# Kernel optimization log

Measured on AMD Instinct MI355X. Metric: run time of the kernel, lower is better.

The kernel has to match this reference:

```python
import jax, jax.numpy as jnp
import numpy as np

N = 100000; E = 800000; IN_DIM = 32; HID = 64; HEADS = 4; HEAD_DIM = HID // HEADS; L = 3; G = 128

def setup_inputs() -> dict:
    key = jax.random.key(0)
    ks = jax.random.split(key, 12)
    nrm = lambda k, shape: jax.random.normal(k, shape, jnp.float32) * 0.05
    return {
        "x": jax.random.normal(ks[0], (N, IN_DIM), jnp.float32),
        "edge_index": jax.random.randint(ks[1], (2, E), 0, N),
        "edge_attr": jax.random.normal(ks[2], (E, 1), jnp.float32),
        "batch": jnp.sort(jax.random.randint(ks[3], (N,), 0, G)),
        "in_W": nrm(ks[4], (IN_DIM, HID)), "in_b": jnp.zeros((HID,), jnp.float32),
        "in_ln_g": jnp.ones((HID,), jnp.float32), "in_ln_b": jnp.zeros((HID,), jnp.float32),
        "W_qkv": nrm(ks[5], (L, 3, HID, HID)), "b_qkv": jnp.zeros((L, 3, HID), jnp.float32),
        "W_edge": nrm(ks[6], (L, 1, HID)),
        "W_skip": nrm(ks[7], (L, HID, HID)), "b_skip": jnp.zeros((L, HID), jnp.float32),
        "W_beta": nrm(ks[8], (L, 3 * HID)),
        "ln_g": jnp.ones((L, HID), jnp.float32), "ln_b": jnp.zeros((L, HID), jnp.float32),
        "r1_W": nrm(ks[9], (2 * HID, HID)), "r1_b": jnp.zeros((HID,), jnp.float32),
        "r2_W": nrm(ks[10], (HID, HID // 2)), "r2_b": jnp.zeros((HID // 2,), jnp.float32),
        "r3_W": nrm(ks[11], (HID // 2, 1)), "r3_b": jnp.zeros((1,), jnp.float32),
    }

def _layer_norm(x, g, b, eps=1e-5):
    mu = x.mean(-1, keepdims=True)
    var = ((x - mu) ** 2).mean(-1, keepdims=True)
    return (x - mu) * jax.lax.rsqrt(var + eps) * g + b

def _gelu(x):
    return jax.nn.gelu(x, approximate=False)  # matches torch F.gelu default (erf)

def _forward(x, edge_attr, in_W, in_b, in_ln_g, in_ln_b, W_qkv, b_qkv, W_edge,
             W_skip, b_skip, W_beta, ln_g, ln_b, r1_W, r1_b, r2_W, r2_b, r3_W, r3_b,
             edge_index, batch):
    src, dst = edge_index[0], edge_index[1]  # message flows src -> dst
    n = x.shape[0]
    h = _layer_norm(_gelu(x @ in_W + in_b), in_ln_g, in_ln_b)
    scale = 1.0 / jnp.sqrt(jnp.float32(HEAD_DIM))
    for l in range(L):
        res = h
        q = (h @ W_qkv[l, 0] + b_qkv[l, 0]).reshape(n, HEADS, HEAD_DIM)
        k = (h @ W_qkv[l, 1] + b_qkv[l, 1]).reshape(n, HEADS, HEAD_DIM)
        v = (h @ W_qkv[l, 2] + b_qkv[l, 2]).reshape(n, HEADS, HEAD_DIM)
        e = (edge_attr @ W_edge[l]).reshape(-1, HEADS, HEAD_DIM)  # [E,H,C]
        ke = k[src] + e
        alpha = jnp.einsum("ehc,ehc->eh", q[dst], ke) * scale      # [E,H]
        amax = jax.ops.segment_max(alpha, dst, num_segments=n)
        ex = jnp.exp(alpha - amax[dst])
        den = jax.ops.segment_sum(ex, dst, num_segments=n)
        alpha = ex / (den[dst] + 1e-16)                            # PyG softmax eps
        msg = alpha[..., None] * (v[src] + e)
        out = jax.ops.segment_sum(msg, dst, num_segments=n).reshape(n, HID)
        x_r = h @ W_skip[l] + b_skip[l]
        beta = jax.nn.sigmoid(jnp.concatenate([out, x_r, out - x_r], -1) @ W_beta[l])  # [N]
        out = beta[:, None] * x_r + (1.0 - beta[:, None]) * out
        h = _layer_norm(_gelu(out) + res, ln_g[l], ln_b[l])
    cnt = jax.ops.segment_sum(jnp.ones((n,), h.dtype), batch, num_segments=G)
    gmean = jax.ops.segment_sum(h, batch, num_segments=G) / jnp.maximum(cnt, 1.0)[:, None]
    gmax = jax.ops.segment_max(h, batch, num_segments=G)
    rep = jnp.concatenate([gmean, gmax], -1)  # [G, 2*HID]
    rep = _gelu(rep @ r1_W + r1_b)
    rep = _gelu(rep @ r2_W + r2_b)
    return (rep @ r3_W + r3_b).reshape(-1)

def reference(x, edge_index, edge_attr, batch, in_W, in_b, in_ln_g, in_ln_b,
              W_qkv, b_qkv, W_edge, W_skip, b_skip, W_beta, ln_g, ln_b,
              r1_W, r1_b, r2_W, r2_b, r3_W, r3_b):
    return _forward(x, edge_attr, in_W, in_b, in_ln_g, in_ln_b, W_qkv, b_qkv, W_edge,
                    W_skip, b_skip, W_beta, ln_g, ln_b, r1_W, r1_b, r2_W, r2_b, r3_W, r3_b,
                    edge_index, batch)
```

## Files before the change

### kernel.cpp

```cpp
#include <hip/hip_runtime.h>
#include <hip/hip_fp16.h>
#include <math.h>
#include <float.h>

#define LAYERS 3
#define NGRAPH 128
#define NPB 1024
#define NBMAX 256

typedef __attribute__((ext_vector_type(8))) short bf16x8;
typedef __attribute__((ext_vector_type(4))) float f32x4;

union bfr { int4 i; bf16x8 b; };

__device__ __forceinline__ float gelu_f(float x) {
    return 0.5f * x * (1.0f + erff(x * 0.70710678118654752440f));
}

template <int CTRL, int RMASK>
__device__ __forceinline__ float dpp_add(float x) {
    int t = __builtin_amdgcn_update_dpp(0, __float_as_int(x), CTRL, RMASK, 0xF, false);
    return x + __int_as_float(t);
}

__device__ __forceinline__ float sum16(float v) {
    v = dpp_add<0xB1, 0xF>(v);
    v = dpp_add<0x4E, 0xF>(v);
    v = dpp_add<0x141, 0xF>(v);
    v = dpp_add<0x140, 0xF>(v);
    return v;
}

__device__ __forceinline__ unsigned int f2mono(float f) {
    unsigned int u = __float_as_uint(f);
    return (u & 0x80000000u) ? ~u : (u | 0x80000000u);
}
__device__ __forceinline__ float mono2f(unsigned int u) {
    return (u & 0x80000000u) ? __uint_as_float(u ^ 0x80000000u)
                             : __uint_as_float(~u);
}

__device__ __forceinline__ float2 h2f2(int bits) {
    __half2 h = *reinterpret_cast<__half2*>(&bits);
    return __half22float2(h);
}

__device__ __forceinline__ void cvt_frag(const float4& f0, const float4& f1,
                                         bf16x8& hi, bf16x8& lo) {
    float ff[8] = {f0.x, f0.y, f0.z, f0.w, f1.x, f1.y, f1.z, f1.w};
#pragma unroll
    for (int j = 0; j < 8; j++) {
        unsigned u = __float_as_uint(ff[j]);
        hi[j] = (short)(u >> 16);
        float hf = __uint_as_float(u & 0xFFFF0000u);
        lo[j] = (short)(__float_as_uint(ff[j] - hf) >> 16);
    }
}

__device__ __forceinline__ f32x4 mm3(const bf16x8& ahi, const bf16x8& alo,
                                     const int4* __restrict__ pk, int tile,
                                     int lane, f32x4 acc) {
    bfr bh, bl;
    bh.i = pk[tile * 128 + lane];
    bl.i = pk[tile * 128 + 64 + lane];
    acc = __builtin_amdgcn_mfma_f32_16x16x32_bf16(alo, bh.b, acc, 0, 0, 0);
    acc = __builtin_amdgcn_mfma_f32_16x16x32_bf16(ahi, bl.b, acc, 0, 0, 0);
    acc = __builtin_amdgcn_mfma_f32_16x16x32_bf16(ahi, bh.b, acc, 0, 0, 0);
    return acc;
}

__device__ __forceinline__ int kv_idx(int m, int cc) {
    return (cc >> 2) * 8 + (m - 1) * 4 + (cc & 3);
}

__global__ __launch_bounds__(256) void k_cvt(
    const float* __restrict__ in_W, const float* __restrict__ W_skip,
    const float* __restrict__ W_qkv, int4* __restrict__ pk_in,
    int4* __restrict__ pk_skip, int4* __restrict__ pk_qkv) {
    int w = (blockIdx.x * 256 + threadIdx.x) >> 6;
    if (w >= 100) return;
    int lane = threadIdx.x & 63;
    const float* src;
    int4* dst;
    int kt, jt, qkvmode = 0;
    if (w < 4) {
        kt = 0; jt = w;
        src = in_W;
        dst = pk_in + w * 128;
    } else {
        int l = (w - 4) >> 5, r = (w - 4) & 31;
        if (r < 8) {
            kt = r & 1; jt = r >> 1;
            src = W_skip + l * 4096;
            dst = pk_skip + (l * 8 + r) * 128;
        } else {
            int tq = r - 8;
            kt = tq & 1; jt = tq >> 1;
            src = W_qkv + l * 12288;
            dst = pk_qkv + (l * 24 + tq) * 128;
            qkvmode = 1;
        }
    }
    int c = jt * 16 + (lane & 15);
    int koff = kt * 32 + (lane >> 4) * 8;
    unsigned hi[8], lo[8];
#pragma unroll
    for (int j = 0; j < 8; j++) {
        int k = koff + j;
        float f = qkvmode ? src[(c >> 6) * 4096 + k * 64 + (c & 63)]
                          : src[k * 64 + c];
        unsigned u = __float_as_uint(f);
        hi[j] = u >> 16;
        float hf = __uint_as_float(u & 0xFFFF0000u);
        lo[j] = __float_as_uint(f - hf) >> 16;
    }
    int4 H, L;
    H.x = hi[0] | (hi[1] << 16); H.y = hi[2] | (hi[3] << 16);
    H.z = hi[4] | (hi[5] << 16); H.w = hi[6] | (hi[7] << 16);
    L.x = lo[0] | (lo[1] << 16); L.y = lo[2] | (lo[3] << 16);
    L.z = lo[4] | (lo[5] << 16); L.w = lo[6] | (lo[7] << 16);
    dst[lane] = H;
    dst[64 + lane] = L;
}

__global__ __launch_bounds__(256) void k_hist(const int* __restrict__ dst,
                                              int* __restrict__ deg, int E) {
    int e = blockIdx.x * 256 + threadIdx.x;
    if (e < E) atomicAdd(&deg[dst[e]], 1);
}

__global__ __launch_bounds__(256) void k_scan1(const int* __restrict__ deg,
                                               int* __restrict__ excl,
                                               int* __restrict__ bsum, int n) {
    __shared__ int s[256];
    int t = threadIdx.x;
    int i = blockIdx.x * 256 + t;
    int v = (i < n) ? deg[i] : 0;
    s[t] = v;
    __syncthreads();
    for (int off = 1; off < 256; off <<= 1) {
        int a = (t >= off) ? s[t - off] : 0;
        __syncthreads();
        s[t] += a;
        __syncthreads();
    }
    if (i < n) excl[i] = s[t] - v;
    if (t == 255) bsum[blockIdx.x] = s[255];
}

__global__ __launch_bounds__(512) void k_scan2(int* __restrict__ bsum, int nb) {
    __shared__ int s[512];
    int t = threadIdx.x;
    int v = (t < nb) ? bsum[t] : 0;
    s[t] = v;
    __syncthreads();
    for (int off = 1; off < 512; off <<= 1) {
        int a = (t >= off) ? s[t - off] : 0;
        __syncthreads();
        s[t] += a;
        __syncthreads();
    }
    if (t < nb) bsum[t] = s[t] - v;
}

__global__ __launch_bounds__(256) void k_scan3(const int* __restrict__ excl,
                                               const int* __restrict__ bsum,
                                               int* __restrict__ row,
                                               int* __restrict__ cursor,
                                               int* __restrict__ gcurb,
                                               int n, int E) {
    int i = blockIdx.x * 256 + threadIdx.x;
    if (i < n) {
        int r = excl[i] + bsum[blockIdx.x];
        row[i] = r;
        cursor[i] = r;
        if ((i & (NPB - 1)) == 0) gcurb[i >> 10] = r;
    }
    if (blockIdx.x == 0 && threadIdx.x == 0) row[n] = E;
}

__global__ __launch_bounds__(256) void k_bucket(
    const int* __restrict__ src, const int* __restrict__ dst,
    const float* __restrict__ ea, int* __restrict__ gcurb,
    int2* __restrict__ mid, int E, int nbkt) {
    __shared__ int cnt[NBMAX], base_[NBMAX];
    int tile = blockIdx.x * 4096;
    for (int i = threadIdx.x; i < nbkt; i += 256) cnt[i] = 0;
    __syncthreads();
    int d[16];
#pragma unroll
    for (int j = 0; j < 16; j++) {
        int e = tile + j * 256 + threadIdx.x;
        d[j] = -1;
        if (e < E) {
            d[j] = dst[e];
            atomicAdd(&cnt[d[j] >> 10], 1);
        }
    }
    __syncthreads();
    for (int i = threadIdx.x; i < nbkt; i += 256) {
        base_[i] = atomicAdd(&gcurb[i], cnt[i]);
        cnt[i] = 0;
    }
    __syncthreads();
#pragma unroll
    for (int j = 0; j < 16; j++) {
        int e = tile + j * 256 + threadIdx.x;
        if (e < E) {
            int b = d[j] >> 10;
            int p = base_[b] + atomicAdd(&cnt[b], 1);
            mid[p] = make_int2(src[e] | ((d[j] & (NPB - 1)) << 20),
                               __float_as_int(ea[e]));
        }
    }
}

__global__ __launch_bounds__(256) void k_local(
    const int* __restrict__ row, int* __restrict__ cursor,
    const int2* __restrict__ mid, int2* __restrict__ ep, int n) {
    int b = blockIdx.x;
    int n0 = b << 10;
    int n1 = min(n, n0 + NPB);
    int ebeg = row[n0], eend = row[n1];
    for (int e = ebeg + blockIdx.y * 256 + threadIdx.x; e < eend;
         e += 256 * gridDim.y) {
        int2 m = mid[e];
        int dn = n0 + ((m.x >> 20) & (NPB - 1));
        int p = atomicAdd(&cursor[dn], 1);
        ep[p] = make_int2(m.x & 0xFFFFF, m.y);
    }
}

__global__ __launch_bounds__(64) void k_in_qkv(
    const float* __restrict__ x, const int4* __restrict__ pk_in,
    const float* __restrict__ b, const float* __restrict__ g,
    const float* __restrict__ be, const int4* __restrict__ pk_qkv,
    const float* __restrict__ bn, float* __restrict__ h,
    __half* __restrict__ q, __half* __restrict__ kvout, int n) {
    __shared__ float ldsA[1088];
    int lane = threadIdx.x;
    int nb = blockIdx.x * 16;
    if (nb >= n) return;
    int g16 = lane >> 4, c16 = lane & 15;
    bool rowok = (nb + c16) < n;
    int arow = min(nb + c16, n - 1);
    const float* xp = x + (size_t)arow * 32 + g16 * 8;
    float4 f0 = *(const float4*)xp;
    float4 f1 = *(const float4*)(xp + 4);
    bf16x8 ahi, alo;
    cvt_frag(f0, f1, ahi, alo);
    float gv[4][4];
#pragma unroll
    for (int jt = 0; jt < 4; jt++) {
        f32x4 a = {0.f, 0.f, 0.f, 0.f};
        a = mm3(ahi, alo, pk_in, jt, lane, a);
        float bb = b[jt * 16 + c16];
#pragma unroll
        for (int r = 0; r < 4; r++) gv[jt][r] = gelu_f(a[r] + bb);
    }
    float gl[4], bel[4];
#pragma unroll
    for (int jt = 0; jt < 4; jt++) {
        gl[jt] = g[jt * 16 + c16];
        bel[jt] = be[jt * 16 + c16];
    }
    float hreg[4][4];
#pragma unroll
    for (int r = 0; r < 4; r++) {
        float s = gv[0][r] + gv[1][r] + gv[2][r] + gv[3][r];
        float mu = sum16(s) * (1.0f / 64.0f);
        float vs = 0.f;
#pragma unroll
        for (int jt = 0; jt < 4; jt++) {
            float d = gv[jt][r] - mu;
            vs += d * d;
        }
        float var = sum16(vs) * (1.0f / 64.0f);
        float rs = rsqrtf(var + 1e-5f);
#pragma unroll
        for (int jt = 0; jt < 4; jt++)
            hreg[jt][r] = (gv[jt][r] - mu) * rs * gl[jt] + bel[jt];
    }
#pragma unroll
    for (int jt = 0; jt < 4; jt++)
#pragma unroll
        for (int r = 0; r < 4; r++)
            ldsA[(g16 * 4 + r) * 68 + jt * 16 + c16] = hreg[jt][r];
    if (rowok) {
        float* hp = h + (size_t)(nb + c16) * 64 + g16 * 16;
#pragma unroll
        for (int i = 0; i < 4; i++)
            *(float4*)(hp + i * 4) = *(const float4*)&ldsA[c16 * 68 + g16 * 16 + i * 4];
    }
    bf16x8 qahi[2], qalo[2];
#pragma unroll
    for (int kt = 0; kt < 2; kt++) {
        const float* lp = &ldsA[c16 * 68 + kt * 32 + g16 * 8];
        float4 t0 = *(const float4*)lp;
        float4 t1 = *(const float4*)(lp + 4);
        cvt_frag(t0, t1, qahi[kt], qalo[kt]);
    }
#pragma unroll
    for (int jt = 0; jt < 12; jt++) {
        f32x4 a = {0.f, 0.f, 0.f, 0.f};
#pragma unroll
        for (int kt = 0; kt < 2; kt++) a = mm3(qahi[kt], qalo[kt], pk_qkv, jt * 2 + kt, lane, a);
        int c = jt * 16 + c16;
        float bias = bn[c];
        int m = c >> 6, cc = c & 63;
#pragma unroll
        for (int r = 0; r < 4; r++) {
            int nd = nb + g16 * 4 + r;
            if (nd < n) {
                float val = a[r] + bias;
                if (m == 0) q[(size_t)nd * 64 + cc] = __float2half(val);
                else kvout[(size_t)nd * 128 + kv_idx(m, cc)] = __float2half(val);
            }
        }
    }
}

__global__ __launch_bounds__(256) void k_attn(
    const __half* __restrict__ q, const __half* __restrict__ kv,
    const int* __restrict__ row, const int2* __restrict__ ep,
    const float* __restrict__ We, float* __restrict__ out, int n) {
    int lane = threadIdx.x & 63;
    int node = blockIdx.x * 4 + (threadIdx.x >> 6);
    if (node >= n) return;
    int g = lane >> 4;
    int c16 = lane & 15;
    int2 qb = *(const int2*)(q + (size_t)node * 64 + c16 * 4);
    float2 q01 = h2f2(qb.x), q23 = h2f2(qb.y);
    float4 wv = *(const float4*)(We + c16 * 4);
    int beg = row[node], end = row[node + 1];
    float den = 0.f;
    float4 acc = {0.f, 0.f, 0.f, 0.f};
    for (int pos = beg; pos < end; pos += 8) {
        int idx0 = pos + g, idx1 = pos + 4 + g;
        bool v0 = idx0 < end, v1 = idx1 < end;
        int2 pr0 = ep[v0 ? idx0 : beg];
        int2 pr1 = ep[v1 ? idx1 : beg];
        float a0 = __int_as_float(pr0.y), a1 = __int_as_float(pr1.y);
        int4 kb0 = *(const int4*)(kv + (size_t)pr0.x * 128 + c16 * 8);
        int4 kb1 = *(const int4*)(kv + (size_t)pr1.x * 128 + c16 * 8);
        {
            float2 k01 = h2f2(kb0.x), k23 = h2f2(kb0.y);
            float2 v01 = h2f2(kb0.z), v23 = h2f2(kb0.w);
            float p = q01.x * fmaf(a0, wv.x, k01.x) + q01.y * fmaf(a0, wv.y, k01.y) +
                      q23.x * fmaf(a0, wv.z, k23.x) + q23.y * fmaf(a0, wv.w, k23.y);
            p = dpp_add<0xB1, 0xF>(p);
            p = dpp_add<0x4E, 0xF>(p);
            float ex = v0 ? __expf(fminf(p * 0.25f, 60.f)) : 0.f;
            den += ex;
            acc.x = fmaf(ex, fmaf(a0, wv.x, v01.x), acc.x);
            acc.y = fmaf(ex, fmaf(a0, wv.y, v01.y), acc.y);
            acc.z = fmaf(ex, fmaf(a0, wv.z, v23.x), acc.z);
            acc.w = fmaf(ex, fmaf(a0, wv.w, v23.y), acc.w);
        }
        {
            float2 k01 = h2f2(kb1.x), k23 = h2f2(kb1.y);
            float2 v01 = h2f2(kb1.z), v23 = h2f2(kb1.w);
            float p = q01.x * fmaf(a1, wv.x, k01.x) + q01.y * fmaf(a1, wv.y, k01.y) +
                      q23.x * fmaf(a1, wv.z, k23.x) + q23.y * fmaf(a1, wv.w, k23.y);
            p = dpp_add<0xB1, 0xF>(p);
            p = dpp_add<0x4E, 0xF>(p);
            float ex = v1 ? __expf(fminf(p * 0.25f, 60.f)) : 0.f;
            den += ex;
            acc.x = fmaf(ex, fmaf(a1, wv.x, v01.x), acc.x);
            acc.y = fmaf(ex, fmaf(a1, wv.y, v01.y), acc.y);
            acc.z = fmaf(ex, fmaf(a1, wv.z, v23.x), acc.z);
            acc.w = fmaf(ex, fmaf(a1, wv.w, v23.y), acc.w);
        }
    }
#pragma unroll
    for (int mask = 16; mask <= 32; mask <<= 1) {
        den += __shfl_xor(den, mask, 64);
        acc.x += __shfl_xor(acc.x, mask, 64);
        acc.y += __shfl_xor(acc.y, mask, 64);
        acc.z += __shfl_xor(acc.z, mask, 64);
        acc.w += __shfl_xor(acc.w, mask, 64);
    }
    if (g == 0) {
        float inv = 1.0f / (den + 1e-16f);
        float4 o = {acc.x * inv, acc.y * inv, acc.z * inv, acc.w * inv};
        *(float4*)(out + (size_t)node * 64 + c16 * 4) = o;
    }
}

template <int DO_QKV>
__global__ __launch_bounds__(64) void k_node_qkv(
    float* __restrict__ h, const float* __restrict__ o_in,
    const int4* __restrict__ pk_skip, const float* __restrict__ bs,
    const float* __restrict__ Wb, const float* __restrict__ lg,
    const float* __restrict__ lb, const int4* __restrict__ pk_qkv,
    const float* __restrict__ bn, __half* __restrict__ q,
    __half* __restrict__ kvout, const int* __restrict__ batch,
    float* __restrict__ gsum, unsigned int* __restrict__ gmaxu,
    float* __restrict__ cnt, int n) {
    __shared__ float ldsA[1088];
    int lane = threadIdx.x;
    int nb = blockIdx.x * 16;
    if (nb >= n) return;
    int g16 = lane >> 4, c16 = lane & 15;
    bool rowok = (nb + c16) < n;
    int arow = min(nb + c16, n - 1);
    float4 hf[2][2];
#pragma unroll
    for (int kt = 0; kt < 2; kt++) {
        const float* hp = h + (size_t)arow * 64 + kt * 32 + g16 * 8;
        hf[kt][0] = *(const float4*)hp;
        hf[kt][1] = *(const float4*)(hp + 4);
    }
    float ov[4][4];
#pragma unroll
    for (int jt = 0; jt < 4; jt++)
#pragma unroll
        for (int r = 0; r < 4; r++) {
            int nd = min(nb + g16 * 4 + r, n - 1);
            ov[jt][r] = o_in[(size_t)nd * 64 + jt * 16 + c16];
        }
    bf16x8 ahi[2], alo[2];
#pragma unroll
    for (int kt = 0; kt < 2; kt++) {
        cvt_frag(hf[kt][0], hf[kt][1], ahi[kt], alo[kt]);
        *(float4*)&ldsA[c16 * 68 + kt * 32 + g16 * 8] = hf[kt][0];
        *(float4*)&ldsA[c16 * 68 + kt * 32 + g16 * 8 + 4] = hf[kt][1];
    }
    float xr[4][4];
#pragma unroll
    for (int jt = 0; jt < 4; jt++) {
        f32x4 a = {0.f, 0.f, 0.f, 0.f};
#pragma unroll
        for (int kt = 0; kt < 2; kt++) a = mm3(ahi[kt], alo[kt], pk_skip, jt * 2 + kt, lane, a);
        float bias = bs[jt * 16 + c16];
#pragma unroll
        for (int r = 0; r < 4; r++) xr[jt][r] = a[r] + bias;
    }
    float hold[4][4];
#pragma unroll
    for (int jt = 0; jt < 4; jt++)
#pragma unroll
        for (int r = 0; r < 4; r++)
            hold[jt][r] = ldsA[(g16 * 4 + r) * 68 + jt * 16 + c16];
    float wb0[4], wb1[4], wb2[4], lgv[4], lbv[4];
#pragma unroll
    for (int jt = 0; jt < 4; jt++) {
        int c = jt * 16 + c16;
        wb0[jt] = Wb[c]; wb1[jt] = Wb[64 + c]; wb2[jt] = Wb[128 + c];
        lgv[jt] = lg[c]; lbv[jt] = lb[c];
    }
    float hnew[4][4];
#pragma unroll
    for (int r = 0; r < 4; r++) {
        float cbs = 0.f;
#pragma unroll
        for (int jt = 0; jt < 4; jt++)
            cbs += ov[jt][r] * wb0[jt] + xr[jt][r] * wb1[jt] +
                   (ov[jt][r] - xr[jt][r]) * wb2[jt];
        float cb = sum16(cbs);
        float beta = 1.0f / (1.0f + expf(-cb));
        float gvr[4], s = 0.f;
#pragma unroll
        for (int jt = 0; jt < 4; jt++) {
            float o2 = fmaf(beta, xr[jt][r] - ov[jt][r], ov[jt][r]);
            gvr[jt] = gelu_f(o2) + hold[jt][r];
            s += gvr[jt];
        }
        float mu = sum16(s) * (1.0f / 64.0f);
        float vs = 0.f;
#pragma unroll
        for (int jt = 0; jt < 4; jt++) {
            float d = gvr[jt] - mu;
            vs += d * d;
        }
        float var = sum16(vs) * (1.0f / 64.0f);
        float rs = rsqrtf(var + 1e-5f);
#pragma unroll
        for (int jt = 0; jt < 4; jt++)
            hnew[jt][r] = (gvr[jt] - mu) * rs * lgv[jt] + lbv[jt];
    }
    if (DO_QKV) {
#pragma unroll
        for (int jt = 0; jt < 4; jt++)
#pragma unroll
            for (int r = 0; r < 4; r++)
                ldsA[(g16 * 4 + r) * 68 + jt * 16 + c16] = hnew[jt][r];
        if (rowok) {
            float* hp = h + (size_t)(nb + c16) * 64 + g16 * 16;
#pragma unroll
            for (int i = 0; i < 4; i++)
                *(float4*)(hp + i * 4) = *(const float4*)&ldsA[c16 * 68 + g16 * 16 + i * 4];
        }
        bf16x8 qahi[2], qalo[2];
#pragma unroll
        for (int kt = 0; kt < 2; kt++) {
            const float* lp = &ldsA[c16 * 68 + kt * 32 + g16 * 8];
            float4 t0 = *(const float4*)lp;
            float4 t1 = *(const float4*)(lp + 4);
            cvt_frag(t0, t1, qahi[kt], qalo[kt]);
        }
#pragma unroll
        for (int jt = 0; jt < 12; jt++) {
            f32x4 a = {0.f, 0.f, 0.f, 0.f};
#pragma unroll
            for (int kt = 0; kt < 2; kt++) a = mm3(qahi[kt], qalo[kt], pk_qkv, jt * 2 + kt, lane, a);
            int c = jt * 16 + c16;
            float bias = bn[c];
            int m = c >> 6, cc = c & 63;
#pragma unroll
            for (int r = 0; r < 4; r++) {
                int nd = nb + g16 * 4 + r;
                if (nd < n) {
                    float val = a[r] + bias;
                    if (m == 0) q[(size_t)nd * 64 + cc] = __float2half(val);
                    else kvout[(size_t)nd * 128 + kv_idx(m, cc)] = __float2half(val);
                }
            }
        }
    } else {
        int gid[4];
        int g0 = batch[nb];
        bool ok = (nb + 15 < n);
#pragma unroll
        for (int r = 0; r < 4; r++)
            gid[r] = batch[min(nb + g16 * 4 + r, n - 1)];
        bool uni = ok && __all(gid[0] == g0 && gid[1] == g0 &&
                               gid[2] == g0 && gid[3] == g0);
        if (uni) {
            float s[4], mx[4];
#pragma unroll
            for (int jt = 0; jt < 4; jt++) {
                s[jt] = hnew[jt][0] + hnew[jt][1] + hnew[jt][2] + hnew[jt][3];
                mx[jt] = fmaxf(fmaxf(hnew[jt][0], hnew[jt][1]),
                               fmaxf(hnew[jt][2], hnew[jt][3]));
            }
#pragma unroll
            for (int mask = 16; mask <= 32; mask <<= 1) {
#pragma unroll
                for (int jt = 0; jt < 4; jt++) {
                    s[jt] += __shfl_xor(s[jt], mask, 64);
                    mx[jt] = fmaxf(mx[jt], __shfl_xor(mx[jt], mask, 64));
                }
            }
            if (g16 == 0) {
#pragma unroll
                for (int jt = 0; jt < 4; jt++) {
                    int ch = jt * 16 + c16;
                    atomicAdd(&gsum[g0 * 64 + ch], s[jt]);
                    atomicMax(&gmaxu[g0 * 64 + ch], f2mono(mx[jt]));
                }
            }
            if (lane == 0) atomicAdd(&cnt[g0], 16.0f);
        } else {
#pragma unroll
            for (int r = 0; r < 4; r++) {
                int nd = nb + g16 * 4 + r;
                if (nd >= n) continue;
#pragma unroll
                for (int jt = 0; jt < 4; jt++) {
                    int ch = jt * 16 + c16;
                    atomicAdd(&gsum[gid[r] * 64 + ch], hnew[jt][r]);
                    atomicMax(&gmaxu[gid[r] * 64 + ch], f2mono(hnew[jt][r]));
                }
                if (c16 == 0) atomicAdd(&cnt[gid[r]], 1.0f);
            }
        }
    }
}

__global__ void k_final(const float* __restrict__ gsum,
                        const unsigned int* __restrict__ gmax,
                        const float* __restrict__ cnt,
                        const float* __restrict__ W1, const float* __restrict__ b1,
                        const float* __restrict__ W2, const float* __restrict__ b2,
                        const float* __restrict__ W3, const float* __restrict__ b3,
                        float* __restrict__ out) {
    int g = blockIdx.x;
    int lane = threadIdx.x;
    __shared__ float rep[128];
    __shared__ float t1[64];
    __shared__ float t2[32];
    float c = fmaxf(cnt[g], 1.0f);
    rep[lane] = gsum[g * 64 + lane] / c;
    rep[64 + lane] = mono2f(gmax[g * 64 + lane]);
    __syncthreads();
    float a = b1[lane];
#pragma unroll 8
    for (int i = 0; i < 128; i++) a = fmaf(rep[i], W1[i * 64 + lane], a);
    t1[lane] = gelu_f(a);
    __syncthreads();
    if (lane < 32) {
        float a2 = b2[lane];
#pragma unroll 8
        for (int i = 0; i < 64; i++) a2 = fmaf(t1[i], W2[i * 32 + lane], a2);
        t2[lane] = gelu_f(a2);
    }
    __syncthreads();
    if (lane < 32) {
        float p = t2[lane] * W3[lane];
#pragma unroll
        for (int o = 16; o > 0; o >>= 1) p += __shfl_xor(p, o, 64);
        if (lane == 0) out[g] = p + b3[0];
    }
}

extern "C" void kernel_launch(void* const* d_in, const int* in_sizes, int n_in,
                              void* d_out, int out_size, void* d_ws,
                              size_t ws_size, hipStream_t stream) {
    const float* x      = (const float*)d_in[0];
    const int*   eidx   = (const int*)d_in[1];
    const float* ea     = (const float*)d_in[2];
    const int*   batch  = (const int*)d_in[3];
    const float* in_W   = (const float*)d_in[4];
    const float* in_b   = (const float*)d_in[5];
    const float* in_lng = (const float*)d_in[6];
    const float* in_lnb = (const float*)d_in[7];
    const float* W_qkv  = (const float*)d_in[8];
    const float* b_qkv  = (const float*)d_in[9];
    const float* W_edge = (const float*)d_in[10];
    const float* W_skip = (const float*)d_in[11];
    const float* b_skip = (const float*)d_in[12];
    const float* W_beta = (const float*)d_in[13];
    const float* ln_g   = (const float*)d_in[14];
    const float* ln_b   = (const float*)d_in[15];
    const float* r1_W   = (const float*)d_in[16];
    const float* r1_b   = (const float*)d_in[17];
    const float* r2_W   = (const float*)d_in[18];
    const float* r2_b   = (const float*)d_in[19];
    const float* r3_W   = (const float*)d_in[20];
    const float* r3_b   = (const float*)d_in[21];

    int n = in_sizes[0] / 32;
    int E = in_sizes[2];
    const int* src = eidx;
    const int* dst = eidx + E;

    char* ws = (char*)d_ws;
    size_t off = 0;
    auto alloc = [&](size_t bytes) -> void* {
        void* p = ws + off;
        off = (off + bytes + 255) & ~(size_t)255;
        return p;
    };
    float* h    = (float*)alloc((size_t)n * 64 * 4);
    __half* qh  = (__half*)alloc((size_t)n * 64 * 2);
    __half* kvh = (__half*)alloc((size_t)n * 128 * 2);
    float* oacc = (float*)alloc((size_t)n * 64 * 4);
    int* deg    = (int*)alloc((size_t)n * 4);
    int* excl   = (int*)alloc((size_t)n * 4);
    int* bsum   = (int*)alloc(512 * 4);
    int* row    = (int*)alloc((size_t)(n + 1) * 4);
    int* cursor = (int*)alloc((size_t)n * 4);
    int* gcurb  = (int*)alloc(NBMAX * 4);
    int2* mid   = (int2*)alloc((size_t)E * 8);
    int2* ep    = (int2*)alloc((size_t)E * 8);
    int4* pk_in   = (int4*)alloc(4 * 128 * 16);
    int4* pk_skip = (int4*)alloc(3 * 8 * 128 * 16);
    int4* pk_qkv  = (int4*)alloc((size_t)3 * 24 * 128 * 16);
    float* gsum = (float*)alloc((NGRAPH * 64 * 2 + NGRAPH) * 4);
    unsigned int* gmaxu = (unsigned int*)(gsum + NGRAPH * 64);
    float* cnt  = gsum + NGRAPH * 128;

    int nb4 = (n + 3) / 4;
    int nb16 = (n + 15) / 16;
    int nbs = (n + 255) / 256;
    int ebs = (E + 255) / 256;
    int nbkt = (n + NPB - 1) >> 10;

    k_cvt<<<25, 256, 0, stream>>>(in_W, W_skip, W_qkv, pk_in, pk_skip, pk_qkv);
    hipMemsetAsync(deg, 0, (size_t)n * 4, stream);
    hipMemsetAsync(gsum, 0, (NGRAPH * 64 * 2 + NGRAPH) * 4, stream);
    k_hist<<<ebs, 256, 0, stream>>>(dst, deg, E);
    k_scan1<<<nbs, 256, 0, stream>>>(deg, excl, bsum, n);
    k_scan2<<<1, 512, 0, stream>>>(bsum, nbs);
    k_scan3<<<nbs, 256, 0, stream>>>(excl, bsum, row, cursor, gcurb, n, E);
    k_bucket<<<(E + 4095) / 4096, 256, 0, stream>>>(src, dst, ea, gcurb, mid, E, nbkt);
    k_local<<<dim3(nbkt, 4), 256, 0, stream>>>(row, cursor, mid, ep, n);

    k_in_qkv<<<nb16, 64, 0, stream>>>(x, pk_in, in_b, in_lng, in_lnb,
                                      pk_qkv, b_qkv, h, qh, kvh, n);

    for (int l = 0; l < LAYERS; l++) {
        k_attn<<<nb4, 256, 0, stream>>>(qh, kvh, row, ep, W_edge + l * 64, oacc, n);
        if (l + 1 < LAYERS) {
            k_node_qkv<1><<<nb16, 64, 0, stream>>>(
                h, oacc, pk_skip + l * 8 * 128, b_skip + l * 64,
                W_beta + l * 192, ln_g + l * 64, ln_b + l * 64,
                pk_qkv + (size_t)(l + 1) * 24 * 128, b_qkv + (size_t)(l + 1) * 192,
                qh, kvh, nullptr, nullptr, nullptr, nullptr, n);
        } else {
            k_node_qkv<0><<<nb16, 64, 0, stream>>>(
                h, oacc, pk_skip + l * 8 * 128, b_skip + l * 64,
                W_beta + l * 192, ln_g + l * 64, ln_b + l * 64,
                nullptr, nullptr, nullptr, nullptr,
                batch, gsum, gmaxu, cnt, n);
        }
    }

    k_final<<<NGRAPH, 64, 0, stream>>>(gsum, gmaxu, cnt, r1_W, r1_b, r2_W, r2_b,
                                       r3_W, r3_b, (float*)d_out);
}
```

Baseline: 385.3 us.

## Stage packed weights in LDS and process four 16-node tiles per block

```diff
diff --git a/kernel.cpp b/kernel.cpp
--- a/kernel.cpp
+++ b/kernel.cpp
@@ -57,12 +57,12 @@
     }
 }
 
-__device__ __forceinline__ f32x4 mm3(const bf16x8& ahi, const bf16x8& alo,
-                                     const int4* __restrict__ pk, int tile,
-                                     int lane, f32x4 acc) {
+__device__ __forceinline__ f32x4 mm3l(const bf16x8& ahi, const bf16x8& alo,
+                                      const int4* wW, int tile, int lane,
+                                      f32x4 acc) {
     bfr bh, bl;
-    bh.i = pk[tile * 128 + lane];
-    bl.i = pk[tile * 128 + 64 + lane];
+    bh.i = wW[tile * 128 + lane];
+    bl.i = wW[tile * 128 + 64 + lane];
     acc = __builtin_amdgcn_mfma_f32_16x16x32_bf16(alo, bh.b, acc, 0, 0, 0);
     acc = __builtin_amdgcn_mfma_f32_16x16x32_bf16(ahi, bl.b, acc, 0, 0, 0);
     acc = __builtin_amdgcn_mfma_f32_16x16x32_bf16(ahi, bh.b, acc, 0, 0, 0);
@@ -231,90 +231,112 @@
     }
 }
 
-__global__ __launch_bounds__(64) void k_in_qkv(
+__global__ __launch_bounds__(256) void k_in_qkv(
     const float* __restrict__ x, const int4* __restrict__ pk_in,
     const float* __restrict__ b, const float* __restrict__ g,
     const float* __restrict__ be, const int4* __restrict__ pk_qkv,
     const float* __restrict__ bn, float* __restrict__ h,
     __half* __restrict__ q, __half* __restrict__ kvout, int n) {
-    __shared__ float ldsA[1088];
-    int lane = threadIdx.x;
-    int nb = blockIdx.x * 16;
-    if (nb >= n) return;
+    __shared__ float ldsA[4][1088];
+    __shared__ int4 wW[1536];
+    int lane = threadIdx.x & 63, wid = threadIdx.x >> 6, tid = threadIdx.x;
+    int nb = (blockIdx.x * 4 + wid) * 16;
+    bool active = nb < n;
     int g16 = lane >> 4, c16 = lane & 15;
-    bool rowok = (nb + c16) < n;
-    int arow = min(nb + c16, n - 1);
-    const float* xp = x + (size_t)arow * 32 + g16 * 8;
-    float4 f0 = *(const float4*)xp;
-    float4 f1 = *(const float4*)(xp + 4);
-    bf16x8 ahi, alo;
-    cvt_frag(f0, f1, ahi, alo);
-    float gv[4][4];
-#pragma unroll
-    for (int jt = 0; jt < 4; jt++) {
-        f32x4 a = {0.f, 0.f, 0.f, 0.f};
-        a = mm3(ahi, alo, pk_in, jt, lane, a);
-        float bb = b[jt * 16 + c16];
-#pragma unroll
-        for (int r = 0; r < 4; r++) gv[jt][r] = gelu_f(a[r] + bb);
-    }
-    float gl[4], bel[4];
-#pragma unroll
-    for (int jt = 0; jt < 4; jt++) {
-        gl[jt] = g[jt * 16 + c16];
-        bel[jt] = be[jt * 16 + c16];
-    }
-    float hreg[4][4];
-#pragma unroll
-    for (int r = 0; r < 4; r++) {
-        float s = gv[0][r] + gv[1][r] + gv[2][r] + gv[3][r];
-        float mu = sum16(s) * (1.0f / 64.0f);
-        float vs = 0.f;
+    bool rowok = active && (nb + c16) < n;
+    int arow = active ? min(nb + c16, n - 1) : 0;
+#pragma unroll
+    for (int i = 0; i < 2; i++) wW[tid + i * 256] = pk_in[tid + i * 256];
+    float4 f0 = {0,0,0,0}, f1 = {0,0,0,0};
+    if (active) {
+        const float* xp = x + (size_t)arow * 32 + g16 * 8;
+        f0 = *(const float4*)xp;
+        f1 = *(const float4*)(xp + 4);
+    }
+    __syncthreads();
+    bf16x8 qahi[2], qalo[2];
+    if (active) {
+        bf16x8 ahi, alo;
+        cvt_frag(f0, f1, ahi, alo);
+        float gv[4][4];
 #pragma unroll
         for (int jt = 0; jt < 4; jt++) {
-            float d = gv[jt][r] - mu;
-            vs += d * d;
-        }
-        float var = sum16(vs) * (1.0f / 64.0f);
-        float rs = rsqrtf(var + 1e-5f);
+            f32x4 a = {0.f, 0.f, 0.f, 0.f};
+            a = mm3l(ahi, alo, wW, jt, lane, a);
+            float bb = b[jt * 16 + c16];
+#pragma unroll
+            for (int r = 0; r < 4; r++) gv[jt][r] = gelu_f(a[r] + bb);
+        }
+        float gl[4], bel[4];
+#pragma unroll
+        for (int jt = 0; jt < 4; jt++) {
+            gl[jt] = g[jt * 16 + c16];
+            bel[jt] = be[jt * 16 + c16];
+        }
+        float hreg[4][4];
+#pragma unroll
+        for (int r = 0; r < 4; r++) {
+            float s = gv[0][r] + gv[1][r] + gv[2][r] + gv[3][r];
+            float mu = sum16(s) * (1.0f / 64.0f);
+            float vs = 0.f;
+#pragma unroll
+            for (int jt = 0; jt < 4; jt++) {
+                float d = gv[jt][r] - mu;
+                vs += d * d;
+            }
+            float var = sum16(vs) * (1.0f / 64.0f);
+            float rs = rsqrtf(var + 1e-5f);
+#pragma unroll
+            for (int jt = 0; jt < 4; jt++)
+                hreg[jt][r] = (gv[jt][r] - mu) * rs * gl[jt] + bel[jt];
+        }
 #pragma unroll
         for (int jt = 0; jt < 4; jt++)
-            hreg[jt][r] = (gv[jt][r] - mu) * rs * gl[jt] + bel[jt];
-    }
-#pragma unroll
-    for (int jt = 0; jt < 4; jt++)
-#pragma unroll
-        for (int r = 0; r < 4; r++)
-            ldsA[(g16 * 4 + r) * 68 + jt * 16 + c16] = hreg[jt][r];
-    if (rowok) {
-        float* hp = h + (size_t)(nb + c16) * 64 + g16 * 16;
-#pragma unroll
-        for (int i = 0; i < 4; i++)
-            *(float4*)(hp + i * 4) = *(const float4*)&ldsA[c16 * 68 + g16 * 16 + i * 4];
-    }
-    bf16x8 qahi[2], qalo[2];
-#pragma unroll
-    for (int kt = 0; kt < 2; kt++) {
-        const float* lp = &ldsA[c16 * 68 + kt * 32 + g16 * 8];
-        float4 t0 = *(const float4*)lp;
-        float4 t1 = *(const float4*)(lp + 4);
-        cvt_frag(t0, t1, qahi[kt], qalo[kt]);
-    }
-#pragma unroll
-    for (int jt = 0; jt < 12; jt++) {
-        f32x4 a = {0.f, 0.f, 0.f, 0.f};
-#pragma unroll
-        for (int kt = 0; kt < 2; kt++) a = mm3(qahi[kt], qalo[kt], pk_qkv, jt * 2 + kt, lane, a);
-        int c = jt * 16 + c16;
-        float bias = bn[c];
-        int m = c >> 6, cc = c & 63;
-#pragma unroll
-        for (int r = 0; r < 4; r++) {
-            int nd = nb + g16 * 4 + r;
-            if (nd < n) {
-                float val = a[r] + bias;
-                if (m == 0) q[(size_t)nd * 64 + cc] = __float2half(val);
-                else kvout[(size_t)nd * 128 + kv_idx(m, cc)] = __float2half(val);
+#pragma unroll
+            for (int r = 0; r < 4; r++)
+                ldsA[wid][(g16 * 4 + r) * 68 + jt * 16 + c16] = hreg[jt][r];
+        if (rowok) {
+            float* hp = h + (size_t)(nb + c16) * 64 + g16 * 16;
+#pragma unroll
+            for (int i = 0; i < 4; i++)
+                *(float4*)(hp + i * 4) =
+                    *(const float4*)&ldsA[wid][c16 * 68 + g16 * 16 + i * 4];
+        }
+#pragma unroll
+        for (int kt = 0; kt < 2; kt++) {
+            const float* lp = &ldsA[wid][c16 * 68 + kt * 32 + g16 * 8];
+            float4 t0 = *(const float4*)lp;
+            float4 t1 = *(const float4*)(lp + 4);
+            cvt_frag(t0, t1, qahi[kt], qalo[kt]);
+        }
+    }
+#pragma unroll
+    for (int half = 0; half < 2; half++) {
+        __syncthreads();
+#pragma unroll
+        for (int i = 0; i < 6; i++)
+            wW[tid + i * 256] = pk_qkv[half * 1536 + tid + i * 256];
+        __syncthreads();
+        if (active) {
+#pragma unroll
+            for (int j6 = 0; j6 < 6; j6++) {
+                int jt = half * 6 + j6;
+                f32x4 a = {0.f, 0.f, 0.f, 0.f};
+#pragma unroll
+                for (int kt = 0; kt < 2; kt++)
+                    a = mm3l(qahi[kt], qalo[kt], wW, j6 * 2 + kt, lane, a);
+                int c = jt * 16 + c16;
+                float bias = bn[c];
+                int m = c >> 6, cc = c & 63;
+#pragma unroll
+                for (int r = 0; r < 4; r++) {
+                    int nd = nb + g16 * 4 + r;
+                    if (nd < n) {
+                        float val = a[r] + bias;
+                        if (m == 0) q[(size_t)nd * 64 + cc] = __float2half(val);
+                        else kvout[(size_t)nd * 128 + kv_idx(m, cc)] = __float2half(val);
+                    }
+                }
             }
         }
     }
@@ -388,7 +410,7 @@
 }
 
 template <int DO_QKV>
-__global__ __launch_bounds__(64) void k_node_qkv(
+__global__ __launch_bounds__(256) void k_node_qkv(
     float* __restrict__ h, const float* __restrict__ o_in,
     const int4* __restrict__ pk_skip, const float* __restrict__ bs,
     const float* __restrict__ Wb, const float* __restrict__ lg,
@@ -397,127 +419,150 @@
     __half* __restrict__ kvout, const int* __restrict__ batch,
     float* __restrict__ gsum, unsigned int* __restrict__ gmaxu,
     float* __restrict__ cnt, int n) {
-    __shared__ float ldsA[1088];
-    int lane = threadIdx.x;
-    int nb = blockIdx.x * 16;
-    if (nb >= n) return;
+    __shared__ float ldsA[4][1088];
+    __shared__ int4 wW[1536];
+    int lane = threadIdx.x & 63, wid = threadIdx.x >> 6, tid = threadIdx.x;
+    int nb = (blockIdx.x * 4 + wid) * 16;
+    bool active = nb < n;
     int g16 = lane >> 4, c16 = lane & 15;
-    bool rowok = (nb + c16) < n;
-    int arow = min(nb + c16, n - 1);
-    float4 hf[2][2];
-#pragma unroll
-    for (int kt = 0; kt < 2; kt++) {
-        const float* hp = h + (size_t)arow * 64 + kt * 32 + g16 * 8;
-        hf[kt][0] = *(const float4*)hp;
-        hf[kt][1] = *(const float4*)(hp + 4);
-    }
+    bool rowok = active && (nb + c16) < n;
+    int arow = active ? min(nb + c16, n - 1) : 0;
+#pragma unroll
+    for (int i = 0; i < 4; i++) wW[tid + i * 256] = pk_skip[tid + i * 256];
+    float4 hf0 = {0,0,0,0}, hf1 = {0,0,0,0}, hf2 = {0,0,0,0}, hf3 = {0,0,0,0};
     float ov[4][4];
-#pragma unroll
-    for (int jt = 0; jt < 4; jt++)
+    if (active) {
+        const float* hp0 = h + (size_t)arow * 64 + g16 * 8;
+        hf0 = *(const float4*)hp0;
+        hf1 = *(const float4*)(hp0 + 4);
+        hf2 = *(const float4*)(hp0 + 32);
+        hf3 = *(const float4*)(hp0 + 36);
+#pragma unroll
+        for (int jt = 0; jt < 4; jt++)
+#pragma unroll
+            for (int r = 0; r < 4; r++) {
+                int nd = min(nb + g16 * 4 + r, n - 1);
+                ov[jt][r] = o_in[(size_t)nd * 64 + jt * 16 + c16];
+            }
+    }
+    __syncthreads();
+    float hnew[4][4];
+    bf16x8 qahi[2], qalo[2];
+    if (active) {
+        bf16x8 ahi[2], alo[2];
+        cvt_frag(hf0, hf1, ahi[0], alo[0]);
+        cvt_frag(hf2, hf3, ahi[1], alo[1]);
+        *(float4*)&ldsA[wid][c16 * 68 + g16 * 8] = hf0;
+        *(float4*)&ldsA[wid][c16 * 68 + g16 * 8 + 4] = hf1;
+        *(float4*)&ldsA[wid][c16 * 68 + 32 + g16 * 8] = hf2;
+        *(float4*)&ldsA[wid][c16 * 68 + 32 + g16 * 8 + 4] = hf3;
+        float xr[4][4];
+#pragma unroll
+        for (int jt = 0; jt < 4; jt++) {
+            f32x4 a = {0.f, 0.f, 0.f, 0.f};
+#pragma unroll
+            for (int kt = 0; kt < 2; kt++)
+                a = mm3l(ahi[kt], alo[kt], wW, jt * 2 + kt, lane, a);
+            float bias = bs[jt * 16 + c16];
+#pragma unroll
+            for (int r = 0; r < 4; r++) xr[jt][r] = a[r] + bias;
+        }
+        float hold[4][4];
+#pragma unroll
+        for (int jt = 0; jt < 4; jt++)
+#pragma unroll
+            for (int r = 0; r < 4; r++)
+                hold[jt][r] = ldsA[wid][(g16 * 4 + r) * 68 + jt * 16 + c16];
+        float wb0[4], wb1[4], wb2[4], lgv[4], lbv[4];
+#pragma unroll
+        for (int jt = 0; jt < 4; jt++) {
+            int c = jt * 16 + c16;
+            wb0[jt] = Wb[c]; wb1[jt] = Wb[64 + c]; wb2[jt] = Wb[128 + c];
+            lgv[jt] = lg[c]; lbv[jt] = lb[c];
+        }
 #pragma unroll
         for (int r = 0; r < 4; r++) {
-            int nd = min(nb + g16 * 4 + r, n - 1);
-            ov[jt][r] = o_in[(size_t)nd * 64 + jt * 16 + c16];
-        }
-    bf16x8 ahi[2], alo[2];
-#pragma unroll
-    for (int kt = 0; kt < 2; kt++) {
-        cvt_frag(hf[kt][0], hf[kt][1], ahi[kt], alo[kt]);
-        *(float4*)&ldsA[c16 * 68 + kt * 32 + g16 * 8] = hf[kt][0];
-        *(float4*)&ldsA[c16 * 68 + kt * 32 + g16 * 8 + 4] = hf[kt][1];
-    }
-    float xr[4][4];
-#pragma unroll
-    for (int jt = 0; jt < 4; jt++) {
-        f32x4 a = {0.f, 0.f, 0.f, 0.f};
-#pragma unroll
-        for (int kt = 0; kt < 2; kt++) a = mm3(ahi[kt], alo[kt], pk_skip, jt * 2 + kt, lane, a);
-        float bias = bs[jt * 16 + c16];
-#pragma unroll
-        for (int r = 0; r < 4; r++) xr[jt][r] = a[r] + bias;
-    }
-    float hold[4][4];
-#pragma unroll
-    for (int jt = 0; jt < 4; jt++)
-#pragma unroll
-        for (int r = 0; r < 4; r++)
-            hold[jt][r] = ldsA[(g16 * 4 + r) * 68 + jt * 16 + c16];
-    float wb0[4], wb1[4], wb2[4], lgv[4], lbv[4];
-#pragma unroll
-    for (int jt = 0; jt < 4; jt++) {
-        int c = jt * 16 + c16;
-        wb0[jt] = Wb[c]; wb1[jt] = Wb[64 + c]; wb2[jt] = Wb[128 + c];
-        lgv[jt] = lg[c]; lbv[jt] = lb[c];
-    }
-    float hnew[4][4];
-#pragma unroll
-    for (int r = 0; r < 4; r++) {
-        float cbs = 0.f;
-#pragma unroll
-        for (int jt = 0; jt < 4; jt++)
-            cbs += ov[jt][r] * wb0[jt] + xr[jt][r] * wb1[jt] +
-                   (ov[jt][r] - xr[jt][r]) * wb2[jt];
-        float cb = sum16(cbs);
-        float beta = 1.0f / (1.0f + expf(-cb));
-        float gvr[4], s = 0.f;
-#pragma unroll
-        for (int jt = 0; jt < 4; jt++) {
-            float o2 = fmaf(beta, xr[jt][r] - ov[jt][r], ov[jt][r]);
-            gvr[jt] = gelu_f(o2) + hold[jt][r];
-            s += gvr[jt];
-        }
-        float mu = sum16(s) * (1.0f / 64.0f);
-        float vs = 0.f;
-#pragma unroll
-        for (int jt = 0; jt < 4; jt++) {
-            float d = gvr[jt] - mu;
-            vs += d * d;
-        }
-        float var = sum16(vs) * (1.0f / 64.0f);
-        float rs = rsqrtf(var + 1e-5f);
-#pragma unroll
-        for (int jt = 0; jt < 4; jt++)
-            hnew[jt][r] = (gvr[jt] - mu) * rs * lgv[jt] + lbv[jt];
+            float cbs = 0.f;
+#pragma unroll
+            for (int jt = 0; jt < 4; jt++)
+                cbs += ov[jt][r] * wb0[jt] + xr[jt][r] * wb1[jt] +
+                       (ov[jt][r] - xr[jt][r]) * wb2[jt];
+            float cb = sum16(cbs);
+            float beta = 1.0f / (1.0f + expf(-cb));
+            float gvr[4], s = 0.f;
+#pragma unroll
+            for (int jt = 0; jt < 4; jt++) {
+                float o2 = fmaf(beta, xr[jt][r] - ov[jt][r], ov[jt][r]);
+                gvr[jt] = gelu_f(o2) + hold[jt][r];
+                s += gvr[jt];
+            }
+            float mu = sum16(s) * (1.0f / 64.0f);
+            float vs = 0.f;
+#pragma unroll
+            for (int jt = 0; jt < 4; jt++) {
+                float d = gvr[jt] - mu;
+                vs += d * d;
+            }
+            float var = sum16(vs) * (1.0f / 64.0f);
+            float rs = rsqrtf(var + 1e-5f);
+#pragma unroll
+            for (int jt = 0; jt < 4; jt++)
+                hnew[jt][r] = (gvr[jt] - mu) * rs * lgv[jt] + lbv[jt];
+        }
+        if (DO_QKV) {
+#pragma unroll
+            for (int jt = 0; jt < 4; jt++)
+#pragma unroll
+                for (int r = 0; r < 4; r++)
+                    ldsA[wid][(g16 * 4 + r) * 68 + jt * 16 + c16] = hnew[jt][r];
+            if (rowok) {
+                float* hp = h + (size_t)(nb + c16) * 64 + g16 * 16;
+#pragma unroll
+                for (int i = 0; i < 4; i++)
+                    *(float4*)(hp + i * 4) =
+                        *(const float4*)&ldsA[wid][c16 * 68 + g16 * 16 + i * 4];
+            }
+#pragma unroll
+            for (int kt = 0; kt < 2; kt++) {
+                const float* lp = &ldsA[wid][c16 * 68 + kt * 32 + g16 * 8];
+                float4 t0 = *(const float4*)lp;
+                float4 t1 = *(const float4*)(lp + 4);
+                cvt_frag(t0, t1, qahi[kt], qalo[kt]);
+            }
+        }
     }
     if (DO_QKV) {
 #pragma unroll
-        for (int jt = 0; jt < 4; jt++)
-#pragma unroll
-            for (int r = 0; r < 4; r++)
-                ldsA[(g16 * 4 + r) * 68 + jt * 16 + c16] = hnew[jt][r];
-        if (rowok) {
-            float* hp = h + (size_t)(nb + c16) * 64 + g16 * 16;
-#pragma unroll
-            for (int i = 0; i < 4; i++)
-                *(float4*)(hp + i * 4) = *(const float4*)&ldsA[c16 * 68 + g16 * 16 + i * 4];
-        }
-        bf16x8 qahi[2], qalo[2];
-#pragma unroll
-        for (int kt = 0; kt < 2; kt++) {
-            const float* lp = &ldsA[c16 * 68 + kt * 32 + g16 * 8];
-            float4 t0 = *(const float4*)lp;
-            float4 t1 = *(const float4*)(lp + 4);
-            cvt_frag(t0, t1, qahi[kt], qalo[kt]);
-        }
-#pragma unroll
-        for (int jt = 0; jt < 12; jt++) {
-            f32x4 a = {0.f, 0.f, 0.f, 0.f};
-#pragma unroll
-            for (int kt = 0; kt < 2; kt++) a = mm3(qahi[kt], qalo[kt], pk_qkv, jt * 2 + kt, lane, a);
-            int c = jt * 16 + c16;
-            float bias = bn[c];
-            int m = c >> 6, cc = c & 63;
-#pragma unroll
-            for (int r = 0; r < 4; r++) {
-                int nd = nb + g16 * 4 + r;
-                if (nd < n) {
-                    float val = a[r] + bias;
-                    if (m == 0) q[(size_t)nd * 64 + cc] = __float2half(val);
-                    else kvout[(size_t)nd * 128 + kv_idx(m, cc)] = __float2half(val);
+        for (int half = 0; half < 2; half++) {
+            __syncthreads();
+#pragma unroll
+            for (int i = 0; i < 6; i++)
+                wW[tid + i * 256] = pk_qkv[half * 1536 + tid + i * 256];
+            __syncthreads();
+            if (active) {
+#pragma unroll
+                for (int j6 = 0; j6 < 6; j6++) {
+                    int jt = half * 6 + j6;
+                    f32x4 a = {0.f, 0.f, 0.f, 0.f};
+#pragma unroll
+                    for (int kt = 0; kt < 2; kt++)
+                        a = mm3l(qahi[kt], qalo[kt], wW, j6 * 2 + kt, lane, a);
+                    int c = jt * 16 + c16;
+                    float bias = bn[c];
+                    int m = c >> 6, cc = c & 63;
+#pragma unroll
+                    for (int r = 0; r < 4; r++) {
+                        int nd = nb + g16 * 4 + r;
+                        if (nd < n) {
+                            float val = a[r] + bias;
+                            if (m == 0) q[(size_t)nd * 64 + cc] = __float2half(val);
+                            else kvout[(size_t)nd * 128 + kv_idx(m, cc)] = __float2half(val);
+                        }
+                    }
                 }
             }
         }
-    } else {
+    } else if (active) {
         int gid[4];
         int g0 = batch[nb];
         bool ok = (nb + 15 < n);
@@ -662,7 +707,7 @@
     float* cnt  = gsum + NGRAPH * 128;
 
     int nb4 = (n + 3) / 4;
-    int nb16 = (n + 15) / 16;
+    int nbB = (n + 63) / 64;
     int nbs = (n + 255) / 256;
     int ebs = (E + 255) / 256;
     int nbkt = (n + NPB - 1) >> 10;
@@ -677,20 +722,20 @@
     k_bucket<<<(E + 4095) / 4096, 256, 0, stream>>>(src, dst, ea, gcurb, mid, E, nbkt);
     k_local<<<dim3(nbkt, 4), 256, 0, stream>>>(row, cursor, mid, ep, n);
 
-    k_in_qkv<<<nb16, 64, 0, stream>>>(x, pk_in, in_b, in_lng, in_lnb,
+    k_in_qkv<<<nbB, 256, 0, stream>>>(x, pk_in, in_b, in_lng, in_lnb,
                                       pk_qkv, b_qkv, h, qh, kvh, n);
 
     for (int l = 0; l < LAYERS; l++) {
         k_attn<<<nb4, 256, 0, stream>>>(qh, kvh, row, ep, W_edge + l * 64, oacc, n);
         if (l + 1 < LAYERS) {
-            k_node_qkv<1><<<nb16, 64, 0, stream>>>(
-                h, oacc, pk_skip + l * 8 * 128, b_skip + l * 64,
+            k_node_qkv<1><<<nbB, 256, 0, stream>>>(
+                h, oacc, pk_skip + l * 1024, b_skip + l * 64,
                 W_beta + l * 192, ln_g + l * 64, ln_b + l * 64,
-                pk_qkv + (size_t)(l + 1) * 24 * 128, b_qkv + (size_t)(l + 1) * 192,
+                pk_qkv + (size_t)(l + 1) * 3072, b_qkv + (size_t)(l + 1) * 192,
                 qh, kvh, nullptr, nullptr, nullptr, nullptr, n);
         } else {
-            k_node_qkv<0><<<nb16, 64, 0, stream>>>(
-                h, oacc, pk_skip + l * 8 * 128, b_skip + l * 64,
+            k_node_qkv<0><<<nbB, 256, 0, stream>>>(
+                h, oacc, pk_skip + l * 1024, b_skip + l * 64,
                 W_beta + l * 192, ln_g + l * 64, ln_b + l * 64,
                 nullptr, nullptr, nullptr, nullptr,
                 batch, gsum, gmaxu, cnt, n);
```

Result: slower. 426.6 us (+10.7%).
